# Kernel tuning notes

Measured on AMD Instinct MI355X. Metric: run time of the kernel, lower is better.

The kernel has to match this reference:

```python
import jax, jax.numpy as jnp
import numpy as np

N = 131072
L = 300  # lan_vec_len

def _boxes(k):
    k1, k2, k3, k4 = jax.random.split(k, 4)
    x1 = jax.random.uniform(k1, (N,)) * 500.0
    y1 = jax.random.uniform(k2, (N,)) * 500.0
    w = 1.0 + jax.random.uniform(k3, (N,)) * 200.0
    h = 1.0 + jax.random.uniform(k4, (N,)) * 200.0
    return x1, y1, x1 + w, y1 + h

def setup_inputs() -> dict:
    key = jax.random.key(0)
    ks = jax.random.split(key, 10)
    sbj_vec = jax.random.normal(ks[0], (N, L), jnp.float32)
    obj_vec = jax.random.normal(ks[1], (N, L), jnp.float32)
    sx1, sy1, sx2, sy2 = _boxes(ks[2])
    ox1, oy1, ox2, oy2 = _boxes(ks[3])
    label = jax.random.randint(ks[4], (N,), 0, 2).astype(jnp.float32)
    misc = jax.random.uniform(ks[5], (N,))
    # rlts columns: [0:4 misc, 4 label, 5:9 sbj box, 9 misc, 10:14 obj box, 14 misc]
    rlts = jnp.stack([misc, misc, misc, misc, label,
                      sx1, sy1, sx2, sy2, misc,
                      ox1, oy1, ox2, oy2, misc], axis=1)
    spa_w = jax.random.normal(ks[6], (8, 1), jnp.float32) * 0.1
    spa_b = jnp.zeros((1,), jnp.float32)
    lan_w1 = jax.random.normal(ks[7], (2 * L, L), jnp.float32) * 0.05
    lan_b1 = jnp.zeros((L,), jnp.float32)
    lan_w2 = jax.random.normal(ks[8], (L, 1), jnp.float32) * 0.05
    lan_b2 = jnp.zeros((1,), jnp.float32)
    return {"sbj_vec": sbj_vec, "obj_vec": obj_vec, "rlts": rlts,
            "spa_w": spa_w, "spa_b": spa_b,
            "lan_w1": lan_w1, "lan_b1": lan_b1,
            "lan_w2": lan_w2, "lan_b2": lan_b2}

def _ext_box_feat(rlts):
    sb = rlts[:, 5:9]
    ob = rlts[:, 10:14]
    sw = sb[:, 2] - sb[:, 0]
    sh = sb[:, 3] - sb[:, 1]
    ow = ob[:, 2] - ob[:, 0]
    oh = ob[:, 3] - ob[:, 1]
    sbj = jnp.stack([(sb[:, 0] - ob[:, 0]) / sw,
                     (sb[:, 1] - ob[:, 1]) / sh,
                     jnp.log(sw / ow), jnp.log(sh / oh)], axis=1)
    obj = jnp.stack([(ob[:, 0] - sb[:, 0]) / ow,
                     (ob[:, 1] - sb[:, 1]) / oh,
                     jnp.log(ow / sw), jnp.log(oh / sh)], axis=1)
    return sbj, obj

def reference(sbj_vec, obj_vec, rlts, spa_w, spa_b, lan_w1, lan_b1, lan_w2, lan_b2):
    sbj_box, obj_box = _ext_box_feat(rlts)
    lan_feat = jnp.concatenate([sbj_vec, obj_vec], axis=1)        # [N, 2L]
    box_feat = jnp.concatenate([sbj_box, obj_box], axis=1)        # [N, 8]
    # lan_stream: ReLU -> (Dropout: identity in eval) -> Linear -> ReLU -> Linear
    h = jax.nn.relu(lan_feat)
    h = jax.nn.relu(h @ lan_w1 + lan_b1)
    lan_scores = h @ lan_w2 + lan_b2                              # [N, 1]
    box_scores = box_feat @ spa_w + spa_b                         # [N, 1]
    scores = jax.nn.sigmoid(lan_scores + box_scores)              # [N, 1]
    ys = (rlts[:, 4] > 0).astype(scores.dtype)                    # [N]
    s = scores[:, 0]
    # binary cross entropy (mean), clamped like torch's BCE
    log_s = jnp.clip(jnp.log(jnp.clip(s, 1e-12, 1.0)), -100.0)
    log_1s = jnp.clip(jnp.log(jnp.clip(1.0 - s, 1e-12, 1.0)), -100.0)
    loss = -jnp.mean(ys * log_s + (1.0 - ys) * log_1s)
    # faithful replication of loss_test's (buggy) counting logic, vectorized
    neg = ys == 0
    pos = ~neg
    N_pos = jnp.sum(pos.astype(jnp.float32))
    N_neg = jnp.sum(neg.astype(jnp.float32))
    N_pos_right = jnp.sum((neg & (s >= 0.5)).astype(jnp.float32))
    N_neg_right = jnp.sum((pos & (s < 0.5)).astype(jnp.float32))
    recall_pos = N_pos_right / N_pos
    recall_neg = N_neg_right / N_neg
    recall_all = (N_pos_right + N_neg_right) / (N_pos + N_neg)
    return scores, loss, recall_pos, recall_neg, recall_all
```

## Files before the change

kernel.cpp:

```cpp
#include <hip/hip_runtime.h>

constexpr int NROWS  = 131072;
constexpr int LDIM   = 300;
constexpr int KDIM   = 600;
constexpr int NPAD   = 320;
constexpr int KGRP   = 76;
constexpr int MTILE  = 64;
constexpr int NBLKS  = NROWS / MTILE;
constexpr int KSTEPS = 19;
constexpr int WT_ELEMS = KGRP * NPAD * 8;
constexpr size_t PART_OFF = 393216;

typedef __bf16 bf16x8 __attribute__((ext_vector_type(8)));
typedef float  f32x4  __attribute__((ext_vector_type(4)));

__device__ __forceinline__ unsigned short f2bf(float f) {
    unsigned u = __float_as_uint(f);
    u += 0x7fffu + ((u >> 16) & 1u);
    return (unsigned short)(u >> 16);
}

__global__ void prep_w1(const float* __restrict__ w1, unsigned short* __restrict__ wt) {
    int idx = blockIdx.x * 256 + threadIdx.x;
    if (idx >= WT_ELEMS) return;
    int j    = idx & 7;
    int rest = idx >> 3;
    int n    = rest % NPAD;
    int kg   = rest / NPAD;
    int k    = kg * 8 + j;
    float v = 0.f;
    if (k < KDIM && n < LDIM) v = w1[k * LDIM + n];
    wt[idx] = f2bf(v);
}

__launch_bounds__(256, 2)
__global__ void main_kernel(const float* __restrict__ sbj, const float* __restrict__ obj,
                            const float* __restrict__ rlts,
                            const float* __restrict__ spa_w, const float* __restrict__ spa_b,
                            const float* __restrict__ b1, const float* __restrict__ w2,
                            const float* __restrict__ b2,
                            const unsigned short* __restrict__ wt,
                            float* __restrict__ out_scores, float* __restrict__ part) {
    __shared__ __attribute__((aligned(16))) unsigned short A_lds[KGRP * MTILE * 8];
    __shared__ float lanpart[4][MTILE];
    __shared__ float redbuf[4][8];

    const int tid  = threadIdx.x;
    const int lane = tid & 63;
    const int wv   = tid >> 6;
    const int l4   = lane & 15;
    const int q4   = lane >> 4;
    const int nbase = wv * 80;

    const int  blk  = blockIdx.x;
    const long row0 = (long)blk * MTILE;

    const int a_quad = tid & 7;
    const int a_row  = tid >> 3;

    #pragma unroll
    for (int kc = 0; kc < KSTEPS; ++kc) {
        const int k0 = kc * 32 + a_quad * 4;
        const int kg = k0 >> 3;
        const int j0 = k0 & 7;
        #pragma unroll
        for (int i = 0; i < 2; ++i) {
            const int  row  = a_row + i * 32;
            const long grow = row0 + row;
            float4 v = make_float4(0.f, 0.f, 0.f, 0.f);
            if (k0 < LDIM)       v = *(const float4*)(sbj + grow * LDIM + k0);
            else if (k0 < KDIM)  v = *(const float4*)(obj + grow * LDIM + (k0 - LDIM));
            unsigned h0 = f2bf(fmaxf(v.x, 0.f));
            unsigned h1 = f2bf(fmaxf(v.y, 0.f));
            unsigned h2 = f2bf(fmaxf(v.z, 0.f));
            unsigned h3 = f2bf(fmaxf(v.w, 0.f));
            uint2 pk = make_uint2(h0 | (h1 << 16), h2 | (h3 << 16));
            *(uint2*)&A_lds[(kg * MTILE + row) * 8 + j0] = pk;
        }
    }

    f32x4 acc[4][5];
    #pragma unroll
    for (int rt = 0; rt < 4; ++rt)
        #pragma unroll
        for (int ct = 0; ct < 5; ++ct)
            acc[rt][ct] = (f32x4)(0.f);

    __syncthreads();

    const int abase = q4 * 512 + l4 * 8;
    const unsigned short* wbase = wt + ((size_t)q4 * NPAD + nbase + l4) * 8;

    #pragma unroll
    for (int kt = 0; kt < KSTEPS; ++kt) {
        bf16x8 af[4];
        #pragma unroll
        for (int rt = 0; rt < 4; ++rt)
            af[rt] = *(const bf16x8*)&A_lds[kt * 2048 + rt * 128 + abase];

        bf16x8 bfr[5];
        #pragma unroll
        for (int ct = 0; ct < 5; ++ct)
            bfr[ct] = *(const bf16x8*)(wbase + (size_t)kt * 4 * NPAD * 8 + ct * 16 * 8);

        #pragma unroll
        for (int ct = 0; ct < 5; ++ct)
            #pragma unroll
            for (int rt = 0; rt < 4; ++rt)
                acc[rt][ct] = __builtin_amdgcn_mfma_f32_16x16x32_bf16(af[rt], bfr[ct], acc[rt][ct], 0, 0, 0);
    }

    float part_r[4][4];
    #pragma unroll
    for (int rt = 0; rt < 4; ++rt)
        #pragma unroll
        for (int r = 0; r < 4; ++r) part_r[rt][r] = 0.f;

    #pragma unroll
    for (int ct = 0; ct < 5; ++ct) {
        const int n = nbase + ct * 16 + l4;
        if (n < LDIM) {
            const float b1n = b1[n];
            const float w2n = w2[n];
            #pragma unroll
            for (int rt = 0; rt < 4; ++rt)
                #pragma unroll
                for (int r = 0; r < 4; ++r) {
                    float h = fmaxf(acc[rt][ct][r] + b1n, 0.f);
                    part_r[rt][r] = fmaf(h, w2n, part_r[rt][r]);
                }
        }
    }
    #pragma unroll
    for (int off = 1; off < 16; off <<= 1)
        #pragma unroll
        for (int rt = 0; rt < 4; ++rt)
            #pragma unroll
            for (int r = 0; r < 4; ++r)
                part_r[rt][r] += __shfl_xor(part_r[rt][r], off, 64);

    if (l4 == 0) {
        #pragma unroll
        for (int rt = 0; rt < 4; ++rt)
            #pragma unroll
            for (int r = 0; r < 4; ++r)
                lanpart[wv][rt * 16 + q4 * 4 + r] = part_r[rt][r];
    }
    __syncthreads();

    float s_loss = 0.f, s_cp = 0.f, s_cn = 0.f, s_pr = 0.f, s_nr = 0.f;
    if (tid < MTILE) {
        const long g   = row0 + tid;
        const float lan = lanpart[0][tid] + lanpart[1][tid] + lanpart[2][tid] + lanpart[3][tid] + b2[0];
        const float* rr = rlts + g * 15;
        const float label = rr[4];
        const float sx1 = rr[5],  sy1 = rr[6],  sx2 = rr[7],  sy2 = rr[8];
        const float ox1 = rr[10], oy1 = rr[11], ox2 = rr[12], oy2 = rr[13];
        const float sw = sx2 - sx1, sh = sy2 - sy1, ow = ox2 - ox1, oh = oy2 - oy1;
        float bs = spa_w[0] * ((sx1 - ox1) / sw)
                 + spa_w[1] * ((sy1 - oy1) / sh)
                 + spa_w[2] * logf(sw / ow)
                 + spa_w[3] * logf(sh / oh)
                 + spa_w[4] * ((ox1 - sx1) / ow)
                 + spa_w[5] * ((oy1 - sy1) / oh)
                 + spa_w[6] * logf(ow / sw)
                 + spa_w[7] * logf(oh / sh)
                 + spa_b[0];
        const float z = lan + bs;
        const float s = 1.f / (1.f + expf(-z));
        out_scores[g] = s;
        const float ls = fmaxf(logf(fminf(fmaxf(s, 1e-12f), 1.f)), -100.f);
        const float l1 = fmaxf(logf(fminf(fmaxf(1.f - s, 1e-12f), 1.f)), -100.f);
        const bool ys = label > 0.f;
        s_loss = ys ? ls : l1;
        s_cp   = ys ? 1.f : 0.f;
        s_cn   = ys ? 0.f : 1.f;
        s_pr   = (!ys && s >= 0.5f) ? 1.f : 0.f;
        s_nr   = (ys && s < 0.5f)  ? 1.f : 0.f;
    }
    #pragma unroll
    for (int off = 1; off < 64; off <<= 1) {
        s_loss += __shfl_xor(s_loss, off, 64);
        s_cp   += __shfl_xor(s_cp, off, 64);
        s_cn   += __shfl_xor(s_cn, off, 64);
        s_pr   += __shfl_xor(s_pr, off, 64);
        s_nr   += __shfl_xor(s_nr, off, 64);
    }
    if (lane == 0) {
        redbuf[wv][0] = s_loss; redbuf[wv][1] = s_cp; redbuf[wv][2] = s_cn;
        redbuf[wv][3] = s_pr;   redbuf[wv][4] = s_nr;
    }
    __syncthreads();
    if (tid == 0) {
        float t0 = 0.f, t1 = 0.f, t2 = 0.f, t3 = 0.f, t4 = 0.f;
        for (int w = 0; w < 4; ++w) {
            t0 += redbuf[w][0]; t1 += redbuf[w][1]; t2 += redbuf[w][2];
            t3 += redbuf[w][3]; t4 += redbuf[w][4];
        }
        part[blk * 8 + 0] = t0; part[blk * 8 + 1] = t1; part[blk * 8 + 2] = t2;
        part[blk * 8 + 3] = t3; part[blk * 8 + 4] = t4;
    }
}

__global__ void final_reduce(const float* __restrict__ part, float* __restrict__ out) {
    __shared__ float red[4][8];
    const int tid = threadIdx.x;
    const int lane = tid & 63, wv = tid >> 6;
    float a0 = 0.f, a1 = 0.f, a2 = 0.f, a3 = 0.f, a4 = 0.f;
    for (int b = tid; b < NBLKS; b += 256) {
        a0 += part[b * 8 + 0]; a1 += part[b * 8 + 1]; a2 += part[b * 8 + 2];
        a3 += part[b * 8 + 3]; a4 += part[b * 8 + 4];
    }
    #pragma unroll
    for (int off = 1; off < 64; off <<= 1) {
        a0 += __shfl_xor(a0, off, 64); a1 += __shfl_xor(a1, off, 64);
        a2 += __shfl_xor(a2, off, 64); a3 += __shfl_xor(a3, off, 64);
        a4 += __shfl_xor(a4, off, 64);
    }
    if (lane == 0) { red[wv][0] = a0; red[wv][1] = a1; red[wv][2] = a2; red[wv][3] = a3; red[wv][4] = a4; }
    __syncthreads();
    if (tid == 0) {
        float t0 = 0.f, t1 = 0.f, t2 = 0.f, t3 = 0.f, t4 = 0.f;
        for (int w = 0; w < 4; ++w) {
            t0 += red[w][0]; t1 += red[w][1]; t2 += red[w][2]; t3 += red[w][3]; t4 += red[w][4];
        }
        out[NROWS + 0] = -t0 / (float)NROWS;
        out[NROWS + 1] = t3 / t1;
        out[NROWS + 2] = t4 / t2;
        out[NROWS + 3] = (t3 + t4) / (t1 + t2);
    }
}

extern "C" void kernel_launch(void* const* d_in, const int* in_sizes, int n_in,
                              void* d_out, int out_size, void* d_ws, size_t ws_size,
                              hipStream_t stream) {
    const float* sbj   = (const float*)d_in[0];
    const float* obj   = (const float*)d_in[1];
    const float* rlts  = (const float*)d_in[2];
    const float* spa_w = (const float*)d_in[3];
    const float* spa_b = (const float*)d_in[4];
    const float* w1    = (const float*)d_in[5];
    const float* b1    = (const float*)d_in[6];
    const float* w2    = (const float*)d_in[7];
    const float* b2    = (const float*)d_in[8];
    float* out = (float*)d_out;

    unsigned short* wt = (unsigned short*)d_ws;
    float* part = (float*)((char*)d_ws + PART_OFF);

    prep_w1<<<(WT_ELEMS + 255) / 256, 256, 0, stream>>>(w1, wt);
    main_kernel<<<NBLKS, 256, 0, stream>>>(sbj, obj, rlts, spa_w, spa_b, b1, w2, b2, wt, out, part);
    final_reduce<<<1, 256, 0, stream>>>(part, out);
}
```

Baseline: 401.4 us.

## Load A fragments directly into registers, each wave owning full N width

Removes the LDS staging of the activation tile. Each wave now loads its 32 rows straight from global memory into MFMA fragment layout, with a register double-buffer prefetch, and computes all 19 column tiles (N padded to 304 instead of 320). Blocks shrink to 128 threads, and the cross-wave reduction of the lane partials is replaced by in-wave shuffles, which drops a barrier and the LDS traffic. In exchange register pressure rises sharply (38 accumulator vectors plus prefetch buffers). Global loads also become less coalesced, since each lane reads 32 contiguous bytes from a different row.

```diff
diff --git a/kernel.cpp b/kernel.cpp
--- a/kernel.cpp
+++ b/kernel.cpp
@@ -3,8 +3,9 @@
 constexpr int NROWS  = 131072;
 constexpr int LDIM   = 300;
 constexpr int KDIM   = 600;
-constexpr int NPAD   = 320;
+constexpr int NPAD   = 304;
 constexpr int KGRP   = 76;
+constexpr int NCT    = 19;
 constexpr int MTILE  = 64;
 constexpr int NBLKS  = NROWS / MTILE;
 constexpr int KSTEPS = 19;
@@ -18,6 +19,15 @@
     unsigned u = __float_as_uint(f);
     u += 0x7fffu + ((u >> 16) & 1u);
     return (unsigned short)(u >> 16);
+}
+
+__device__ __forceinline__ bf16x8 cvt8(const float4& a, const float4& b) {
+    union { uint4 u; bf16x8 v; } r;
+    r.u.x = (unsigned)f2bf(fmaxf(a.x, 0.f)) | ((unsigned)f2bf(fmaxf(a.y, 0.f)) << 16);
+    r.u.y = (unsigned)f2bf(fmaxf(a.z, 0.f)) | ((unsigned)f2bf(fmaxf(a.w, 0.f)) << 16);
+    r.u.z = (unsigned)f2bf(fmaxf(b.x, 0.f)) | ((unsigned)f2bf(fmaxf(b.y, 0.f)) << 16);
+    r.u.w = (unsigned)f2bf(fmaxf(b.z, 0.f)) | ((unsigned)f2bf(fmaxf(b.w, 0.f)) << 16);
+    return r.v;
 }
 
 __global__ void prep_w1(const float* __restrict__ w1, unsigned short* __restrict__ wt) {
@@ -33,7 +43,7 @@
     wt[idx] = f2bf(v);
 }
 
-__launch_bounds__(256, 2)
+__launch_bounds__(128, 2)
 __global__ void main_kernel(const float* __restrict__ sbj, const float* __restrict__ obj,
                             const float* __restrict__ rlts,
                             const float* __restrict__ spa_w, const float* __restrict__ spa_b,
@@ -41,117 +51,126 @@
                             const float* __restrict__ b2,
                             const unsigned short* __restrict__ wt,
                             float* __restrict__ out_scores, float* __restrict__ part) {
-    __shared__ __attribute__((aligned(16))) unsigned short A_lds[KGRP * MTILE * 8];
-    __shared__ float lanpart[4][MTILE];
-    __shared__ float redbuf[4][8];
+    __shared__ float redbuf[2][8];
 
     const int tid  = threadIdx.x;
     const int lane = tid & 63;
     const int wv   = tid >> 6;
     const int l4   = lane & 15;
     const int q4   = lane >> 4;
-    const int nbase = wv * 80;
-
-    const int  blk  = blockIdx.x;
-    const long row0 = (long)blk * MTILE;
-
-    const int a_quad = tid & 7;
-    const int a_row  = tid >> 3;
-
-    #pragma unroll
-    for (int kc = 0; kc < KSTEPS; ++kc) {
-        const int k0 = kc * 32 + a_quad * 4;
-        const int kg = k0 >> 3;
-        const int j0 = k0 & 7;
-        #pragma unroll
-        for (int i = 0; i < 2; ++i) {
-            const int  row  = a_row + i * 32;
-            const long grow = row0 + row;
-            float4 v = make_float4(0.f, 0.f, 0.f, 0.f);
-            if (k0 < LDIM)       v = *(const float4*)(sbj + grow * LDIM + k0);
-            else if (k0 < KDIM)  v = *(const float4*)(obj + grow * LDIM + (k0 - LDIM));
-            unsigned h0 = f2bf(fmaxf(v.x, 0.f));
-            unsigned h1 = f2bf(fmaxf(v.y, 0.f));
-            unsigned h2 = f2bf(fmaxf(v.z, 0.f));
-            unsigned h3 = f2bf(fmaxf(v.w, 0.f));
-            uint2 pk = make_uint2(h0 | (h1 << 16), h2 | (h3 << 16));
-            *(uint2*)&A_lds[(kg * MTILE + row) * 8 + j0] = pk;
-        }
-    }
-
-    f32x4 acc[4][5];
-    #pragma unroll
-    for (int rt = 0; rt < 4; ++rt)
-        #pragma unroll
-        for (int ct = 0; ct < 5; ++ct)
+
+    const int  blk   = blockIdx.x;
+    const long wrow0 = (long)blk * MTILE + (long)wv * 32;
+
+    const float* sb[2];
+    const float* ob[2];
+    #pragma unroll
+    for (int rt = 0; rt < 2; ++rt) {
+        const long r = wrow0 + rt * 16 + l4;
+        sb[rt] = sbj + r * (long)LDIM + q4 * 8;
+        ob[rt] = obj + r * (long)LDIM + q4 * 8 - LDIM;
+    }
+    const unsigned short* bb = wt + ((size_t)q4 * NPAD + l4) * 8;
+
+    f32x4 acc[2][NCT];
+    #pragma unroll
+    for (int rt = 0; rt < 2; ++rt)
+        #pragma unroll
+        for (int ct = 0; ct < NCT; ++ct)
             acc[rt][ct] = (f32x4)(0.f);
 
-    __syncthreads();
-
-    const int abase = q4 * 512 + l4 * 8;
-    const unsigned short* wbase = wt + ((size_t)q4 * NPAD + nbase + l4) * 8;
+    float4 ar[2][2][2];
+
+    auto ldA = [&](int kt, int slot) {
+        #pragma unroll
+        for (int rt = 0; rt < 2; ++rt) {
+            const int kf = kt * 32 + q4 * 8;
+            float4 va, vb;
+            if (kf < LDIM)          va = *(const float4*)(sb[rt] + kt * 32);
+            else if (kf < KDIM)     va = *(const float4*)(ob[rt] + kt * 32);
+            else                    va = make_float4(0.f, 0.f, 0.f, 0.f);
+            if (kf + 4 < LDIM)      vb = *(const float4*)(sb[rt] + kt * 32 + 4);
+            else if (kf + 4 < KDIM) vb = *(const float4*)(ob[rt] + kt * 32 + 4);
+            else                    vb = make_float4(0.f, 0.f, 0.f, 0.f);
+            ar[slot][rt][0] = va;
+            ar[slot][rt][1] = vb;
+        }
+    };
+
+    ldA(0, 0);
 
     #pragma unroll
     for (int kt = 0; kt < KSTEPS; ++kt) {
-        bf16x8 af[4];
-        #pragma unroll
-        for (int rt = 0; rt < 4; ++rt)
-            af[rt] = *(const bf16x8*)&A_lds[kt * 2048 + rt * 128 + abase];
-
-        bf16x8 bfr[5];
-        #pragma unroll
-        for (int ct = 0; ct < 5; ++ct)
-            bfr[ct] = *(const bf16x8*)(wbase + (size_t)kt * 4 * NPAD * 8 + ct * 16 * 8);
-
-        #pragma unroll
-        for (int ct = 0; ct < 5; ++ct)
-            #pragma unroll
-            for (int rt = 0; rt < 4; ++rt)
-                acc[rt][ct] = __builtin_amdgcn_mfma_f32_16x16x32_bf16(af[rt], bfr[ct], acc[rt][ct], 0, 0, 0);
-    }
-
-    float part_r[4][4];
-    #pragma unroll
-    for (int rt = 0; rt < 4; ++rt)
-        #pragma unroll
-        for (int r = 0; r < 4; ++r) part_r[rt][r] = 0.f;
-
-    #pragma unroll
-    for (int ct = 0; ct < 5; ++ct) {
-        const int n = nbase + ct * 16 + l4;
+        const int slot = kt & 1;
+        if (kt + 1 < KSTEPS) ldA(kt + 1, slot ^ 1);
+
+        bf16x8 af[2];
+        af[0] = cvt8(ar[slot][0][0], ar[slot][0][1]);
+        af[1] = cvt8(ar[slot][1][0], ar[slot][1][1]);
+
+        const unsigned short* bk = bb + (size_t)kt * 4 * NPAD * 8;
+
+        bf16x8 bfr[10];
+        #pragma unroll
+        for (int c = 0; c < 10; ++c) bfr[c] = *(const bf16x8*)(bk + c * 128);
+        #pragma unroll
+        for (int c = 0; c < 10; ++c) {
+            acc[0][c] = __builtin_amdgcn_mfma_f32_16x16x32_bf16(af[0], bfr[c], acc[0][c], 0, 0, 0);
+            acc[1][c] = __builtin_amdgcn_mfma_f32_16x16x32_bf16(af[1], bfr[c], acc[1][c], 0, 0, 0);
+        }
+        #pragma unroll
+        for (int c = 0; c < 9; ++c) bfr[c] = *(const bf16x8*)(bk + (10 + c) * 128);
+        #pragma unroll
+        for (int c = 0; c < 9; ++c) {
+            acc[0][10 + c] = __builtin_amdgcn_mfma_f32_16x16x32_bf16(af[0], bfr[c], acc[0][10 + c], 0, 0, 0);
+            acc[1][10 + c] = __builtin_amdgcn_mfma_f32_16x16x32_bf16(af[1], bfr[c], acc[1][10 + c], 0, 0, 0);
+        }
+    }
+
+    float pr[2][4];
+    #pragma unroll
+    for (int rt = 0; rt < 2; ++rt)
+        #pragma unroll
+        for (int r = 0; r < 4; ++r) pr[rt][r] = 0.f;
+
+    #pragma unroll
+    for (int ct = 0; ct < NCT; ++ct) {
+        const int n = ct * 16 + l4;
         if (n < LDIM) {
             const float b1n = b1[n];
             const float w2n = w2[n];
             #pragma unroll
-            for (int rt = 0; rt < 4; ++rt)
+            for (int rt = 0; rt < 2; ++rt)
                 #pragma unroll
                 for (int r = 0; r < 4; ++r) {
                     float h = fmaxf(acc[rt][ct][r] + b1n, 0.f);
-                    part_r[rt][r] = fmaf(h, w2n, part_r[rt][r]);
+                    pr[rt][r] = fmaf(h, w2n, pr[rt][r]);
                 }
         }
     }
     #pragma unroll
     for (int off = 1; off < 16; off <<= 1)
         #pragma unroll
-        for (int rt = 0; rt < 4; ++rt)
+        for (int rt = 0; rt < 2; ++rt)
             #pragma unroll
             for (int r = 0; r < 4; ++r)
-                part_r[rt][r] += __shfl_xor(part_r[rt][r], off, 64);
-
-    if (l4 == 0) {
-        #pragma unroll
-        for (int rt = 0; rt < 4; ++rt)
-            #pragma unroll
-            for (int r = 0; r < 4; ++r)
-                lanpart[wv][rt * 16 + q4 * 4 + r] = part_r[rt][r];
-    }
-    __syncthreads();
+                pr[rt][r] += __shfl_xor(pr[rt][r], off, 64);
+
+    const int t   = lane;
+    const int src = ((t >> 2) & 3) << 4;
+    const float a00 = __shfl(pr[0][0], src, 64), a01 = __shfl(pr[0][1], src, 64);
+    const float a02 = __shfl(pr[0][2], src, 64), a03 = __shfl(pr[0][3], src, 64);
+    const float a10 = __shfl(pr[1][0], src, 64), a11 = __shfl(pr[1][1], src, 64);
+    const float a12 = __shfl(pr[1][2], src, 64), a13 = __shfl(pr[1][3], src, 64);
+    const int rs = t & 3;
+    const float v0 = (rs == 0) ? a00 : (rs == 1) ? a01 : (rs == 2) ? a02 : a03;
+    const float v1 = (rs == 0) ? a10 : (rs == 1) ? a11 : (rs == 2) ? a12 : a13;
+    const float lanraw = ((t >> 4) & 1) ? v1 : v0;
 
     float s_loss = 0.f, s_cp = 0.f, s_cn = 0.f, s_pr = 0.f, s_nr = 0.f;
-    if (tid < MTILE) {
-        const long g   = row0 + tid;
-        const float lan = lanpart[0][tid] + lanpart[1][tid] + lanpart[2][tid] + lanpart[3][tid] + b2[0];
+    if (t < 32) {
+        const long g   = wrow0 + t;
+        const float lan = lanraw + b2[0];
         const float* rr = rlts + g * 15;
         const float label = rr[4];
         const float sx1 = rr[5],  sy1 = rr[6],  sx2 = rr[7],  sy2 = rr[8];
@@ -193,7 +212,7 @@
     __syncthreads();
     if (tid == 0) {
         float t0 = 0.f, t1 = 0.f, t2 = 0.f, t3 = 0.f, t4 = 0.f;
-        for (int w = 0; w < 4; ++w) {
+        for (int w = 0; w < 2; ++w) {
             t0 += redbuf[w][0]; t1 += redbuf[w][1]; t2 += redbuf[w][2];
             t3 += redbuf[w][3]; t4 += redbuf[w][4];
         }
@@ -249,6 +268,6 @@
     float* part = (float*)((char*)d_ws + PART_OFF);
 
     prep_w1<<<(WT_ELEMS + 255) / 256, 256, 0, stream>>>(w1, wt);
-    main_kernel<<<NBLKS, 256, 0, stream>>>(sbj, obj, rlts, spa_w, spa_b, b1, w2, b2, wt, out, part);
+    main_kernel<<<NBLKS, 128, 0, stream>>>(sbj, obj, rlts, spa_w, spa_b, b1, w2, b2, wt, out, part);
     final_reduce<<<1, 256, 0, stream>>>(part, out);
 }
```

After: 473.8 us. +18.0%, slower.
